# Kernel tuning notes

Measured on AMD Instinct MI355X. Metric: run time of the kernel, lower is better.

Reference implementation:

```python
import jax, jax.numpy as jnp
import numpy as np

T, H, E, K = 4096, 1024, 8, 2
DFF = 4 * H
EPS = 1e-9


def setup_inputs() -> dict:
    key = jax.random.key(0)
    ks = jax.random.split(key, 16)
    s = 0.02
    return {
        "x":   jax.random.normal(ks[0], (T, H), jnp.float32),
        # backbone Linear(H,H)
        "Wb":  jax.random.normal(ks[1], (H, H), jnp.float32) * s,
        "bb":  jnp.zeros((H,), jnp.float32),
        # gate Linear(H,E)
        "Wg":  jax.random.normal(ks[2], (H, E), jnp.float32) * s,
        # stacked expert FFN weights: H -> 4H -> H
        "W1":  jax.random.normal(ks[3], (E, H, DFF), jnp.float32) * s,
        "b1":  jnp.zeros((E, DFF), jnp.float32),
        "W2":  jax.random.normal(ks[4], (E, DFF, H), jnp.float32) * s,
        "b2":  jnp.zeros((E, H), jnp.float32),
        # residual expert (same architecture, separate weights)
        "Wr1": jax.random.normal(ks[5], (H, DFF), jnp.float32) * s,
        "br1": jnp.zeros((DFF,), jnp.float32),
        "Wr2": jax.random.normal(ks[6], (DFF, H), jnp.float32) * s,
        "br2": jnp.zeros((H,), jnp.float32),
        # residual mixing coefficient Linear(H,2)
        "Wc":  jax.random.normal(ks[7], (H, 2), jnp.float32) * s,
        "bc":  jnp.zeros((2,), jnp.float32),
        # classification head Linear(H,10)
        "Wh":  jax.random.normal(ks[8], (H, 10), jnp.float32) * s,
        "bh":  jnp.zeros((10,), jnp.float32),
    }


def reference(x, Wb, bb, Wg, W1, b1, W2, b2, Wr1, br1, Wr2, br2, Wc, bc, Wh, bh):
    # backbone MLP
    h = jax.nn.relu(x @ Wb + bb)                                  # [T,H]

    # --- gating: softmax over experts, top-k selection, renormalize ---
    gates = jax.nn.softmax(h @ Wg, axis=-1)                       # [T,E]
    topv, topi = jax.lax.top_k(gates, K)                          # [T,K]
    topw = topv / (jnp.sum(topv, axis=-1, keepdims=True) + EPS)   # [T,K]
    sel = jax.nn.one_hot(topi, E, dtype=h.dtype)                  # [T,K,E]
    w = jnp.einsum("tk,tke->te", topw, sel)                       # [T,E] sparse combine weights

    # load-balancing aux loss (top-1 assignment fraction vs mean gate prob)
    me = jnp.mean(gates, axis=0)                                  # [E]
    ce = jnp.mean(sel[:, 0, :], axis=0)                           # [E]
    l_aux = jnp.sum(me * ce) * E

    # --- expert FFNs (dense all-expert reference) + weighted combine ---
    mid = jax.nn.relu(jnp.einsum("th,ehf->tef", h, W1) + b1)      # [T,E,4H]
    eout = jnp.einsum("tef,efh->teh", mid, W2) + b2               # [T,E,H]
    moe_out = jnp.einsum("te,teh->th", w, eout)                   # [T,H]

    # --- residual expert branch with learned mixing coefficient ---
    res = jax.nn.relu(h @ Wr1 + br1) @ Wr2 + br2                  # [T,H]
    coef = jax.nn.softmax(h @ Wc + bc, axis=-1)                   # [T,2]
    out = moe_out * coef[:, 0:1] + res * coef[:, 1:2]             # [T,H]

    logits = out @ Wh + bh                                        # [T,10]
    return logits, l_aux
```

## Files before the change

### kernel.cpp

```cpp
#include <hip/hip_runtime.h>

typedef unsigned short u16;
typedef unsigned int   u32;
typedef __attribute__((ext_vector_type(8))) __bf16 bf16x8;
typedef __attribute__((ext_vector_type(4))) float  f32x4;

#define TT   4096
#define HD   1024
#define NE   8
#define DF   4096
#define NROW 12288

#define OFF_XCAT   ((size_t)0)
#define OFF_WBCAT  (OFF_XCAT  + 25165824)
#define OFF_W1T    (OFF_WBCAT + 6291456)
#define OFF_W2T    (OFF_W1T   + 75497472)
#define OFF_B1S    (OFF_W2T   + 75497472)
#define OFF_B2S    (OFF_B1S   + 147456)
#define OFF_H32    (OFF_B2S   + 36864)
#define OFF_HBF    (OFF_H32   + 16777216)
#define OFF_HPERM  (OFF_HBF   + 8388608)
#define OFF_MID    (OFF_HPERM + 25165824)
#define OFF_EOUT   (OFF_MID   + 100663296)
#define OFF_TOKA   (OFF_EOUT  + 50331648)
#define OFF_TOKB   (OFF_TOKA  + 65536)
#define OFF_META   (OFF_TOKB  + 65536)

__device__ __forceinline__ u16 f2bf(float f) {
  u32 u = __builtin_bit_cast(u32, f);
  u += 0x7fffu + ((u >> 16) & 1u);
  return (u16)(u >> 16);
}
__device__ __forceinline__ float bf2f(u16 h) {
  u32 u = ((u32)h) << 16;
  return __builtin_bit_cast(float, u);
}
__device__ __forceinline__ u32 pack2(u16 a, u16 b) {
  return (u32)a | ((u32)b << 16);
}


__global__ __launch_bounds__(256) void xcat_kernel(const float* __restrict__ x,
                                                   u16* __restrict__ out) {
  int idx8 = (blockIdx.x * 256 + threadIdx.x) * 8;
  int t = idx8 >> 10, k = idx8 & 1023;
  float v[8];
  *(float4*)&v[0] = *(const float4*)(x + idx8);
  *(float4*)&v[4] = *(const float4*)(x + idx8 + 4);
  u16 hi[8], lo[8];
  #pragma unroll
  for (int j = 0; j < 8; ++j) {
    hi[j] = f2bf(v[j]);
    lo[j] = f2bf(v[j] - bf2f(hi[j]));
  }
  uint4 HI = make_uint4(pack2(hi[0], hi[1]), pack2(hi[2], hi[3]),
                        pack2(hi[4], hi[5]), pack2(hi[6], hi[7]));
  uint4 LO = make_uint4(pack2(lo[0], lo[1]), pack2(lo[2], lo[3]),
                        pack2(lo[4], lo[5]), pack2(lo[6], lo[7]));
  size_t rb = (size_t)t * 3072 + k;
  *(uint4*)&out[rb]        = HI;
  *(uint4*)&out[rb + 1024] = HI;
  *(uint4*)&out[rb + 2048] = LO;
}

__global__ __launch_bounds__(256) void wbcat_kernel(const float* __restrict__ Wb,
                                                    u16* __restrict__ out) {
  __shared__ float tile[64][65];
  int c0 = blockIdx.x * 64, r0 = blockIdx.y * 64;
  int tx = threadIdx.x & 63, ty = threadIdx.x >> 6;
  #pragma unroll
  for (int j = 0; j < 16; ++j) {
    int r = ty + j * 4;
    tile[r][tx] = Wb[(size_t)(r0 + r) * HD + c0 + tx];
  }
  __syncthreads();
  int lane = threadIdx.x & 63, wid = threadIdx.x >> 6;
  int q = lane & 7, cc = lane >> 3;
  #pragma unroll
  for (int h = 0; h < 2; ++h) {
    int c = h * 32 + wid * 8 + cc;
    int rb = q * 8;
    u16 hi[8], lo[8];
    #pragma unroll
    for (int j = 0; j < 8; ++j) {
      float w = tile[rb + j][c];
      hi[j] = f2bf(w);
      lo[j] = f2bf(w - bf2f(hi[j]));
    }
    uint4 HI = make_uint4(pack2(hi[0], hi[1]), pack2(hi[2], hi[3]),
                          pack2(hi[4], hi[5]), pack2(hi[6], hi[7]));
    uint4 LO = make_uint4(pack2(lo[0], lo[1]), pack2(lo[2], lo[3]),
                          pack2(lo[4], lo[5]), pack2(lo[6], lo[7]));
    size_t ob = (size_t)(c0 + c) * 3072 + r0 + rb;
    *(uint4*)&out[ob]        = HI;
    *(uint4*)&out[ob + 1024] = LO;
    *(uint4*)&out[ob + 2048] = HI;
  }
}

__global__ __launch_bounds__(256) void transpose_cvt(const float* __restrict__ Wmain,
                                                     const float* __restrict__ Wres,
                                                     u16* __restrict__ out,
                                                     int R, int C) {
  __shared__ float tile[64][65];
  int e = blockIdx.z;
  const float* in = (e < 8) ? (Wmain + (size_t)e * R * C) : Wres;
  u16* o = out + (size_t)e * R * C;
  int c0 = blockIdx.x * 64, r0 = blockIdx.y * 64;
  int tx = threadIdx.x & 63, ty = threadIdx.x >> 6;
  #pragma unroll
  for (int j = 0; j < 16; ++j) {
    int r = ty + j * 4;
    tile[r][tx] = in[(size_t)(r0 + r) * C + c0 + tx];
  }
  __syncthreads();
  int lane = threadIdx.x & 63, wid = threadIdx.x >> 6;
  int q = lane & 7, cc = lane >> 3;
  #pragma unroll
  for (int h = 0; h < 2; ++h) {
    int c = h * 32 + wid * 8 + cc;
    int rb = q * 8;
    u16 b[8];
    #pragma unroll
    for (int j = 0; j < 8; ++j) b[j] = f2bf(tile[rb + j][c]);
    uint4 P = make_uint4(pack2(b[0], b[1]), pack2(b[2], b[3]),
                         pack2(b[4], b[5]), pack2(b[6], b[7]));
    *(uint4*)&o[(size_t)(c0 + c) * R + r0 + rb] = P;
  }
}

__global__ __launch_bounds__(256) void prep_kernel(const float* __restrict__ b1,
                                                   const float* __restrict__ br1,
                                                   const float* __restrict__ b2,
                                                   const float* __restrict__ br2,
                                                   float* __restrict__ b1s,
                                                   float* __restrict__ b2s,
                                                   int* __restrict__ cnt,
                                                   int* __restrict__ off,
                                                   float* __restrict__ me,
                                                   float* __restrict__ ce) {
  int idx = blockIdx.x * 256 + threadIdx.x;
  if (idx < 36864) {
    b1s[idx] = (idx < 32768) ? b1[idx] : br1[idx - 32768];
  } else if (idx < 46080) {
    int j = idx - 36864;
    b2s[j] = (j < 8192) ? b2[j] : br2[j - 8192];
  } else if (idx < 46144) {
    int j = idx - 46080;
    if (j < 16) cnt[j] = 0;
    else if (j < 32) off[j - 16] = 0;
    else if (j < 40) me[j - 32] = 0.f;
    else if (j < 48) ce[j - 40] = 0.f;
  }
}

template <int RELU, int OUTF32, int OUTBF16, int SWAP>
__global__ __launch_bounds__(256) void gemm_bt(const u16* __restrict__ A,
                                               const u16* __restrict__ BT,
                                               const float* __restrict__ bias,
                                               float* __restrict__ Cf,
                                               u16* __restrict__ Cb,
                                               const int* __restrict__ off,
                                               int M, int K, int N) {
  __shared__ u16 As[128 * 64];
  __shared__ u16 Bs[128 * 64];
  const int z = blockIdx.z;
  const int bx = SWAP ? blockIdx.y : blockIdx.x;
  const int by = SWAP ? blockIdx.x : blockIdx.y;
  int base, cntr;
  if (off) { base = off[z]; cntr = off[z + 1] - base; }
  else     { base = 0;      cntr = M; }
  if (by * 128 >= cntr) return;

  const int tid = threadIdx.x, lane = tid & 63, wid = tid >> 6;
  const int wm = wid & 1, wn = wid >> 1;
  const u16* Bz = BT + (size_t)z * N * K;
  const int r8 = lane >> 3;
  const int c8 = (lane & 7) ^ r8;
  const int colb = c8 * 8;

  f32x4 acc[4][4] = {};

  const int kiters = K >> 6;
  for (int kt = 0; kt < kiters; ++kt) {
    #pragma unroll
    for (int i = 0; i < 4; ++i) {
      int rt = wid * 32 + i * 8 + r8;
      int lr = by * 128 + rt;
      lr = lr < cntr ? lr : cntr - 1;
      const u16* ga = A + (size_t)(base + lr) * K + kt * 64 + colb;
      __builtin_amdgcn_global_load_lds(
          (const __attribute__((address_space(1))) void*)ga,
          (__attribute__((address_space(3))) void*)&As[(wid * 32 + i * 8) * 64],
          16, 0, 0);
      int nn = bx * 128 + rt;
      const u16* gb = Bz + (size_t)nn * K + kt * 64 + colb;
      __builtin_amdgcn_global_load_lds(
          (const __attribute__((address_space(1))) void*)gb,
          (__attribute__((address_space(3))) void*)&Bs[(wid * 32 + i * 8) * 64],
          16, 0, 0);
    }
    __syncthreads();
    {
      const int rsel = lane & 15, quad = lane >> 4;
      const int rr = rsel & 7, rhi = rsel >> 3;
      #pragma unroll
      for (int kk = 0; kk < 2; ++kk) {
        const int sc = (kk * 4 + quad) ^ rr;
        bf16x8 af[4], bfr[4];
        #pragma unroll
        for (int mt = 0; mt < 4; ++mt) {
          int slab = wm * 8 + mt * 2 + rhi;
          af[mt] = *(const bf16x8*)&As[slab * 512 + rr * 64 + sc * 8];
        }
        #pragma unroll
        for (int nt = 0; nt < 4; ++nt) {
          int slab = wn * 8 + nt * 2 + rhi;
          bfr[nt] = *(const bf16x8*)&Bs[slab * 512 + rr * 64 + sc * 8];
        }
        #pragma unroll
        for (int mt = 0; mt < 4; ++mt)
          #pragma unroll
          for (int nt = 0; nt < 4; ++nt)
            acc[mt][nt] = __builtin_amdgcn_mfma_f32_16x16x32_bf16(
                af[mt], bfr[nt], acc[mt][nt], 0, 0, 0);
      }
    }
    __syncthreads();
  }

  const int rq = (lane >> 4) * 4, cq = lane & 15;
  #pragma unroll
  for (int nt = 0; nt < 4; ++nt) {
    int gc = bx * 128 + wn * 64 + nt * 16 + cq;
    float bv = bias ? bias[(size_t)z * N + gc] : 0.f;
    #pragma unroll
    for (int mt = 0; mt < 4; ++mt) {
      #pragma unroll
      for (int i = 0; i < 4; ++i) {
        int rt = wm * 64 + mt * 16 + rq + i;
        int lr = by * 128 + rt;
        if (lr < cntr) {
          float v = acc[mt][nt][i] + bv;
          if (RELU) v = fmaxf(v, 0.f);
          size_t idx = (size_t)(base + lr) * N + gc;
          if (OUTF32)  Cf[idx] = v;
          if (OUTBF16) Cb[idx] = f2bf(v);
        }
      }
    }
  }
}

__global__ __launch_bounds__(256) void gating_kernel(const float* __restrict__ h32,
                                                     const float* __restrict__ Wg,
                                                     const float* __restrict__ Wc,
                                                     const float* __restrict__ bc,
                                                     int4* __restrict__ tokA,
                                                     float4* __restrict__ tokB,
                                                     float* __restrict__ me,
                                                     float* __restrict__ ce,
                                                     int* __restrict__ cnt) {
  __shared__ float lme[8];
  __shared__ float lce[8];
  int tid = threadIdx.x, lane = tid & 63, wid = tid >> 6;
  if (tid < 8) { lme[tid] = 0.f; lce[tid] = 0.f; }
  __syncthreads();

  int t = blockIdx.x * 4 + wid;
  const float* hr = h32 + (size_t)t * HD;
  float g[8] = {0, 0, 0, 0, 0, 0, 0, 0};
  float c0 = 0.f, c1 = 0.f;
  for (int cc = 0; cc < 4; ++cc) {
    int k0 = cc * 256 + lane * 4;
    float hv[4];
    *(float4*)hv = *(const float4*)(hr + k0);
    #pragma unroll
    for (int i = 0; i < 4; ++i) {
      float hx = hv[i];
      const float4* wg = (const float4*)(Wg + (size_t)(k0 + i) * 8);
      float4 w0 = wg[0], w1 = wg[1];
      g[0] += hx * w0.x; g[1] += hx * w0.y; g[2] += hx * w0.z; g[3] += hx * w0.w;
      g[4] += hx * w1.x; g[5] += hx * w1.y; g[6] += hx * w1.z; g[7] += hx * w1.w;
      float2 wc = *(const float2*)(Wc + (size_t)(k0 + i) * 2);
      c0 += hx * wc.x; c1 += hx * wc.y;
    }
  }
  #pragma unroll
  for (int s = 32; s > 0; s >>= 1) {
    #pragma unroll
    for (int e = 0; e < 8; ++e) g[e] += __shfl_down(g[e], s);
    c0 += __shfl_down(c0, s);
    c1 += __shfl_down(c1, s);
  }
  if (lane == 0) {
    float m = g[0];
    #pragma unroll
    for (int e = 1; e < 8; ++e) m = fmaxf(m, g[e]);
    float ex[8], ssum = 0.f;
    #pragma unroll
    for (int e = 0; e < 8; ++e) { ex[e] = expf(g[e] - m); ssum += ex[e]; }
    float inv = 1.f / ssum;
    float ge[8];
    #pragma unroll
    for (int e = 0; e < 8; ++e) ge[e] = ex[e] * inv;
    float v0 = -1.f, v1 = -1.f; int i0 = 0, i1 = 0;
    #pragma unroll
    for (int e = 0; e < 8; ++e) {
      float v = ge[e];
      if (v > v0)      { v1 = v0; i1 = i0; v0 = v; i0 = e; }
      else if (v > v1) { v1 = v; i1 = e; }
    }
    float wsum = v0 + v1 + 1e-9f;
    float w0 = v0 / wsum, w1 = v1 / wsum;
    float ca = c0 + bc[0], cb = c1 + bc[1];
    float mm = fmaxf(ca, cb);
    float e0 = expf(ca - mm), e1 = expf(cb - mm);
    float cinv = 1.f / (e0 + e1);
    int r0 = atomicAdd(&cnt[i0], 1);
    int r1 = atomicAdd(&cnt[i1], 1);
    tokA[t] = make_int4(i0, i1, r0, r1);
    tokB[t] = make_float4(w0, w1, e0 * cinv, e1 * cinv);
    #pragma unroll
    for (int e = 0; e < 8; ++e) atomicAdd(&lme[e], ge[e]);
    atomicAdd(&lce[i0], 1.f);
  }
  __syncthreads();
  if (tid < 8) { atomicAdd(&me[tid], lme[tid]); atomicAdd(&ce[tid], lce[tid]); }
}

__global__ void scan_kernel(const int* __restrict__ cnt, int* __restrict__ off,
                            const float* __restrict__ me, const float* __restrict__ ce,
                            float* __restrict__ laux) {
  if (threadIdx.x == 0) {
    int o = 0;
    for (int e = 0; e < 8; ++e) { off[e] = o; o += cnt[e]; }
    off[8] = o;
    off[9] = o + TT;
    float s = 0.f;
    for (int e = 0; e < 8; ++e) s += me[e] * ce[e];
    laux[0] = s * 8.f / ((float)TT * (float)TT);
  }
}

__global__ __launch_bounds__(256) void scatter_kernel(const u16* __restrict__ hbf,
                                                      u16* __restrict__ hperm,
                                                      const int4* __restrict__ tokA,
                                                      const int* __restrict__ off) {
  int t = blockIdx.x, tid = threadIdx.x;
  int4 a = tokA[t];
  size_t p0 = (size_t)(off[a.x] + a.z) * HD;
  size_t p1 = (size_t)(off[a.y] + a.w) * HD;
  size_t pr = (size_t)(8192 + t) * HD;
  uint2 v = ((const uint2*)(hbf + (size_t)t * HD))[tid];
  ((uint2*)(hperm + p0))[tid] = v;
  ((uint2*)(hperm + p1))[tid] = v;
  ((uint2*)(hperm + pr))[tid] = v;
}

__global__ __launch_bounds__(256) void combine_head(const float* __restrict__ eout,
                                                    const int4* __restrict__ tokA,
                                                    const float4* __restrict__ tokB,
                                                    const int* __restrict__ off,
                                                    const float* __restrict__ Wh,
                                                    const float* __restrict__ bh,
                                                    float* __restrict__ logits) {
  int tid = threadIdx.x, lane = tid & 63, wid = tid >> 6;
  int t = blockIdx.x * 4 + wid;
  int4 a = tokA[t];
  float4 b = tokB[t];
  const float* p0 = eout + (size_t)(off[a.x] + a.z) * HD;
  const float* p1 = eout + (size_t)(off[a.y] + a.w) * HD;
  const float* pr = eout + (size_t)(8192 + t) * HD;
  float acc[10] = {};
  for (int cc = 0; cc < 4; ++cc) {
    int k0 = cc * 256 + lane * 4;
    float v0[4], v1[4], vr[4];
    *(float4*)v0 = *(const float4*)(p0 + k0);
    *(float4*)v1 = *(const float4*)(p1 + k0);
    *(float4*)vr = *(const float4*)(pr + k0);
    #pragma unroll
    for (int i = 0; i < 4; ++i) {
      float outv = b.z * (b.x * v0[i] + b.y * v1[i]) + b.w * vr[i];
      const float* wr = Wh + (size_t)(k0 + i) * 10;
      #pragma unroll
      for (int j = 0; j < 10; ++j) acc[j] += outv * wr[j];
    }
  }
  #pragma unroll
  for (int s = 32; s > 0; s >>= 1) {
    #pragma unroll
    for (int j = 0; j < 10; ++j) acc[j] += __shfl_down(acc[j], s);
  }
  if (lane == 0) {
    #pragma unroll
    for (int j = 0; j < 10; ++j) logits[(size_t)t * 10 + j] = acc[j] + bh[j];
  }
}

extern "C" void kernel_launch(void* const* d_in, const int* in_sizes, int n_in,
                              void* d_out, int out_size, void* d_ws, size_t ws_size,
                              hipStream_t stream) {
  const float* x   = (const float*)d_in[0];
  const float* Wb  = (const float*)d_in[1];
  const float* bb  = (const float*)d_in[2];
  const float* Wg  = (const float*)d_in[3];
  const float* W1  = (const float*)d_in[4];
  const float* b1  = (const float*)d_in[5];
  const float* W2  = (const float*)d_in[6];
  const float* b2  = (const float*)d_in[7];
  const float* Wr1 = (const float*)d_in[8];
  const float* br1 = (const float*)d_in[9];
  const float* Wr2 = (const float*)d_in[10];
  const float* br2 = (const float*)d_in[11];
  const float* Wc  = (const float*)d_in[12];
  const float* bc  = (const float*)d_in[13];
  const float* Wh  = (const float*)d_in[14];
  const float* bh  = (const float*)d_in[15];
  float* out = (float*)d_out;

  char* w = (char*)d_ws;
  u16*    xcat  = (u16*)(w + OFF_XCAT);
  u16*    wbcat = (u16*)(w + OFF_WBCAT);
  u16*    w1t   = (u16*)(w + OFF_W1T);
  u16*    w2t   = (u16*)(w + OFF_W2T);
  float*  b1s   = (float*)(w + OFF_B1S);
  float*  b2s   = (float*)(w + OFF_B2S);
  float*  h32   = (float*)(w + OFF_H32);
  u16*    hbf   = (u16*)(w + OFF_HBF);
  u16*    hperm = (u16*)(w + OFF_HPERM);
  u16*    mid   = (u16*)(w + OFF_MID);
  float*  eout  = (float*)(w + OFF_EOUT);
  int4*   tokA  = (int4*)(w + OFF_TOKA);
  float4* tokB  = (float4*)(w + OFF_TOKB);
  int*    cnt   = (int*)(w + OFF_META);
  int*    off   = cnt + 16;
  float*  me    = (float*)(off + 16);
  float*  ce    = me + 8;

  xcat_kernel<<<dim3(2048), dim3(256), 0, stream>>>(x, xcat);
  wbcat_kernel<<<dim3(16, 16), dim3(256), 0, stream>>>(Wb, wbcat);
  transpose_cvt<<<dim3(64, 16, 9), dim3(256), 0, stream>>>(W1, Wr1, w1t, 1024, 4096);
  transpose_cvt<<<dim3(16, 64, 9), dim3(256), 0, stream>>>(W2, Wr2, w2t, 4096, 1024);
  prep_kernel<<<dim3(181), dim3(256), 0, stream>>>(b1, br1, b2, br2, b1s, b2s, cnt, off, me, ce);

  gemm_bt<1, 1, 1, 0><<<dim3(8, 32, 1), dim3(256), 0, stream>>>(
      xcat, wbcat, bb, h32, hbf, (const int*)nullptr, 4096, 3072, 1024);

  gating_kernel<<<dim3(1024), dim3(256), 0, stream>>>(h32, Wg, Wc, bc, tokA, tokB, me, ce, cnt);
  scan_kernel<<<dim3(1), dim3(64), 0, stream>>>(cnt, off, me, ce, out + 40960);
  scatter_kernel<<<dim3(4096), dim3(256), 0, stream>>>(hbf, hperm, tokA, off);

  gemm_bt<1, 0, 1, 0><<<dim3(32, 32, 9), dim3(256), 0, stream>>>(
      hperm, w1t, b1s, (float*)nullptr, mid, off, 0, 1024, 4096);
  gemm_bt<0, 1, 0, 1><<<dim3(32, 8, 9), dim3(256), 0, stream>>>(
      mid, w2t, b2s, eout, (u16*)nullptr, off, 0, 4096, 1024);

  combine_head<<<dim3(1024), dim3(256), 0, stream>>>(eout, tokA, tokB, off, Wh, bh, out);
}
```

Before: 1.062 ms.

## Split-K the backbone and second expert GEMMs into two partial buffers

Adds a KSPLIT template parameter so the backbone GEMM and the second expert GEMM each split their K loop into two halves, written to separate fp32 buffers. The partial sums are added in a new relu_cast kernel for the backbone, and inside combine_head for the expert outputs. This doubles the grid to improve occupancy on low-block-count GEMMs, at the cost of extra fp32 partial writes and reads. Dead workspace regions (xcat, eout) are reused as partial buffers. The old SWAP grid mapping for the W2 GEMM is dropped.

```diff
diff --git a/kernel.cpp b/kernel.cpp
--- a/kernel.cpp
+++ b/kernel.cpp
@@ -154,27 +154,30 @@
   }
 }
 
-template <int RELU, int OUTF32, int OUTBF16, int SWAP>
+template <int RELU, int OUTF32, int OUTBF16, int KSPLIT>
 __global__ __launch_bounds__(256) void gemm_bt(const u16* __restrict__ A,
                                                const u16* __restrict__ BT,
                                                const float* __restrict__ bias,
                                                float* __restrict__ Cf,
+                                               float* __restrict__ Cf1,
                                                u16* __restrict__ Cb,
                                                const int* __restrict__ off,
                                                int M, int K, int N) {
   __shared__ u16 As[128 * 64];
   __shared__ u16 Bs[128 * 64];
-  const int z = blockIdx.z;
-  const int bx = SWAP ? blockIdx.y : blockIdx.x;
-  const int by = SWAP ? blockIdx.x : blockIdx.y;
+  const int zz = blockIdx.z;
+  const int expert = (KSPLIT > 1) ? (zz / KSPLIT) : zz;
+  const int kchunk = (KSPLIT > 1) ? (zz % KSPLIT) : 0;
+  const int bx = blockIdx.x;
+  const int by = blockIdx.y;
   int base, cntr;
-  if (off) { base = off[z]; cntr = off[z + 1] - base; }
-  else     { base = 0;      cntr = M; }
+  if (off) { base = off[expert]; cntr = off[expert + 1] - base; }
+  else     { base = 0;           cntr = M; }
   if (by * 128 >= cntr) return;
 
   const int tid = threadIdx.x, lane = tid & 63, wid = tid >> 6;
   const int wm = wid & 1, wn = wid >> 1;
-  const u16* Bz = BT + (size_t)z * N * K;
+  const u16* Bz = BT + (size_t)expert * N * K;
   const int r8 = lane >> 3;
   const int c8 = (lane & 7) ^ r8;
   const int colb = c8 * 8;
@@ -182,7 +185,9 @@
   f32x4 acc[4][4] = {};
 
   const int kiters = K >> 6;
-  for (int kt = 0; kt < kiters; ++kt) {
+  const int kspan = kiters / KSPLIT;
+  const int kbeg = kchunk * kspan, kend = kbeg + kspan;
+  for (int kt = kbeg; kt < kend; ++kt) {
     #pragma unroll
     for (int i = 0; i < 4; ++i) {
       int rt = wid * 32 + i * 8 + r8;
@@ -229,11 +234,12 @@
     __syncthreads();
   }
 
+  float* __restrict__ dstF = (KSPLIT > 1 && kchunk) ? Cf1 : Cf;
   const int rq = (lane >> 4) * 4, cq = lane & 15;
   #pragma unroll
   for (int nt = 0; nt < 4; ++nt) {
     int gc = bx * 128 + wn * 64 + nt * 16 + cq;
-    float bv = bias ? bias[(size_t)z * N + gc] : 0.f;
+    float bv = (bias && kchunk == 0) ? bias[(size_t)expert * N + gc] : 0.f;
     #pragma unroll
     for (int mt = 0; mt < 4; ++mt) {
       #pragma unroll
@@ -244,12 +250,36 @@
           float v = acc[mt][nt][i] + bv;
           if (RELU) v = fmaxf(v, 0.f);
           size_t idx = (size_t)(base + lr) * N + gc;
-          if (OUTF32)  Cf[idx] = v;
+          if (OUTF32)  dstF[idx] = v;
           if (OUTBF16) Cb[idx] = f2bf(v);
         }
       }
     }
   }
+}
+
+__global__ __launch_bounds__(256) void relu_cast(const float* __restrict__ pa,
+                                                 const float* __restrict__ pb,
+                                                 float* __restrict__ h32,
+                                                 u16* __restrict__ hbf) {
+  int i8 = (blockIdx.x * 256 + threadIdx.x) * 8;
+  float a[8], b[8];
+  *(float4*)&a[0] = *(const float4*)(pa + i8);
+  *(float4*)&a[4] = *(const float4*)(pa + i8 + 4);
+  *(float4*)&b[0] = *(const float4*)(pb + i8);
+  *(float4*)&b[4] = *(const float4*)(pb + i8 + 4);
+  u16 p[8];
+  float v[8];
+  #pragma unroll
+  for (int j = 0; j < 8; ++j) {
+    v[j] = fmaxf(a[j] + b[j], 0.f);
+    p[j] = f2bf(v[j]);
+  }
+  *(float4*)(h32 + i8)     = *(float4*)&v[0];
+  *(float4*)(h32 + i8 + 4) = *(float4*)&v[4];
+  uint4 P = make_uint4(pack2(p[0], p[1]), pack2(p[2], p[3]),
+                       pack2(p[4], p[5]), pack2(p[6], p[7]));
+  *(uint4*)&hbf[i8] = P;
 }
 
 __global__ __launch_bounds__(256) void gating_kernel(const float* __restrict__ h32,
@@ -358,7 +388,8 @@
   ((uint2*)(hperm + pr))[tid] = v;
 }
 
-__global__ __launch_bounds__(256) void combine_head(const float* __restrict__ eout,
+__global__ __launch_bounds__(256) void combine_head(const float* __restrict__ eoutA,
+                                                    const float* __restrict__ eoutB,
                                                     const int4* __restrict__ tokA,
                                                     const float4* __restrict__ tokB,
                                                     const int* __restrict__ off,
@@ -369,19 +400,25 @@
   int t = blockIdx.x * 4 + wid;
   int4 a = tokA[t];
   float4 b = tokB[t];
-  const float* p0 = eout + (size_t)(off[a.x] + a.z) * HD;
-  const float* p1 = eout + (size_t)(off[a.y] + a.w) * HD;
-  const float* pr = eout + (size_t)(8192 + t) * HD;
+  size_t r0 = (size_t)(off[a.x] + a.z) * HD;
+  size_t r1 = (size_t)(off[a.y] + a.w) * HD;
+  size_t rr = (size_t)(8192 + t) * HD;
   float acc[10] = {};
   for (int cc = 0; cc < 4; ++cc) {
     int k0 = cc * 256 + lane * 4;
-    float v0[4], v1[4], vr[4];
-    *(float4*)v0 = *(const float4*)(p0 + k0);
-    *(float4*)v1 = *(const float4*)(p1 + k0);
-    *(float4*)vr = *(const float4*)(pr + k0);
+    float v0a[4], v1a[4], vra[4], v0b[4], v1b[4], vrb[4];
+    *(float4*)v0a = *(const float4*)(eoutA + r0 + k0);
+    *(float4*)v1a = *(const float4*)(eoutA + r1 + k0);
+    *(float4*)vra = *(const float4*)(eoutA + rr + k0);
+    *(float4*)v0b = *(const float4*)(eoutB + r0 + k0);
+    *(float4*)v1b = *(const float4*)(eoutB + r1 + k0);
+    *(float4*)vrb = *(const float4*)(eoutB + rr + k0);
     #pragma unroll
     for (int i = 0; i < 4; ++i) {
-      float outv = b.z * (b.x * v0[i] + b.y * v1[i]) + b.w * vr[i];
+      float e0 = v0a[i] + v0b[i];
+      float e1 = v1a[i] + v1b[i];
+      float er = vra[i] + vrb[i];
+      float outv = b.z * (b.x * e0 + b.y * e1) + b.w * er;
       const float* wr = Wh + (size_t)(k0 + i) * 10;
       #pragma unroll
       for (int j = 0; j < 10; ++j) acc[j] += outv * wr[j];
@@ -426,17 +463,19 @@
   u16*    w2t   = (u16*)(w + OFF_W2T);
   float*  b1s   = (float*)(w + OFF_B1S);
   float*  b2s   = (float*)(w + OFF_B2S);
-  float*  h32   = (float*)(w + OFF_H32);
+  float*  h32a  = (float*)(w + OFF_H32);
   u16*    hbf   = (u16*)(w + OFF_HBF);
   u16*    hperm = (u16*)(w + OFF_HPERM);
   u16*    mid   = (u16*)(w + OFF_MID);
-  float*  eout  = (float*)(w + OFF_EOUT);
+  float*  eoutA = (float*)(w + OFF_EOUT);
   int4*   tokA  = (int4*)(w + OFF_TOKA);
   float4* tokB  = (float4*)(w + OFF_TOKB);
   int*    cnt   = (int*)(w + OFF_META);
   int*    off   = cnt + 16;
   float*  me    = (float*)(off + 16);
   float*  ce    = me + 8;
+  float*  h32b  = (float*)(w + OFF_EOUT);
+  float*  eoutB = (float*)(w + OFF_XCAT);
 
   xcat_kernel<<<dim3(2048), dim3(256), 0, stream>>>(x, xcat);
   wbcat_kernel<<<dim3(16, 16), dim3(256), 0, stream>>>(Wb, wbcat);
@@ -444,17 +483,18 @@
   transpose_cvt<<<dim3(16, 64, 9), dim3(256), 0, stream>>>(W2, Wr2, w2t, 4096, 1024);
   prep_kernel<<<dim3(181), dim3(256), 0, stream>>>(b1, br1, b2, br2, b1s, b2s, cnt, off, me, ce);
 
-  gemm_bt<1, 1, 1, 0><<<dim3(8, 32, 1), dim3(256), 0, stream>>>(
-      xcat, wbcat, bb, h32, hbf, (const int*)nullptr, 4096, 3072, 1024);
-
-  gating_kernel<<<dim3(1024), dim3(256), 0, stream>>>(h32, Wg, Wc, bc, tokA, tokB, me, ce, cnt);
+  gemm_bt<0, 1, 0, 2><<<dim3(8, 32, 2), dim3(256), 0, stream>>>(
+      xcat, wbcat, bb, h32a, h32b, (u16*)nullptr, (const int*)nullptr, 4096, 3072, 1024);
+  relu_cast<<<dim3(2048), dim3(256), 0, stream>>>(h32a, h32b, h32a, hbf);
+
+  gating_kernel<<<dim3(1024), dim3(256), 0, stream>>>(h32a, Wg, Wc, bc, tokA, tokB, me, ce, cnt);
   scan_kernel<<<dim3(1), dim3(64), 0, stream>>>(cnt, off, me, ce, out + 40960);
   scatter_kernel<<<dim3(4096), dim3(256), 0, stream>>>(hbf, hperm, tokA, off);
 
-  gemm_bt<1, 0, 1, 0><<<dim3(32, 32, 9), dim3(256), 0, stream>>>(
-      hperm, w1t, b1s, (float*)nullptr, mid, off, 0, 1024, 4096);
-  gemm_bt<0, 1, 0, 1><<<dim3(32, 8, 9), dim3(256), 0, stream>>>(
-      mid, w2t, b2s, eout, (u16*)nullptr, off, 0, 4096, 1024);
-
-  combine_head<<<dim3(1024), dim3(256), 0, stream>>>(eout, tokA, tokB, off, Wh, bh, out);
-}
+  gemm_bt<1, 0, 1, 1><<<dim3(32, 32, 9), dim3(256), 0, stream>>>(
+      hperm, w1t, b1s, (float*)nullptr, (float*)nullptr, mid, off, 0, 1024, 4096);
+  gemm_bt<0, 1, 0, 2><<<dim3(8, 32, 18), dim3(256), 0, stream>>>(
+      mid, w2t, b2s, eoutA, eoutB, (u16*)nullptr, off, 0, 4096, 1024);
+
+  combine_head<<<dim3(1024), dim3(256), 0, stream>>>(eoutA, eoutB, tokA, tokB, off, Wh, bh, out);
+}
```

New measurement: 913.5 us. 1.16x faster.
